# Performance work log

Hardware: AMD Instinct MI355X
Metric: run time of the kernel (lower is better)

Reference implementation:

```python
import jax, jax.numpy as jnp
import numpy as np

B, S, E, H = 1024, 64, 1024, 16  # batch, seq (n_agent+1), n_embd, num_heads
D = E // H  # head_dim = 64


def setup_inputs() -> dict:
    k = jax.random.key(0)
    ks = jax.random.split(k, 7)
    w = lambda i: jax.random.normal(ks[i], (E, E), jnp.float32) * 0.02
    return {
        "query": jax.random.normal(ks[0], (B, S, E), jnp.float32),
        "key": jax.random.normal(ks[1], (B, S, E), jnp.float32),
        "value": jax.random.normal(ks[2], (B, S, E), jnp.float32),
        "Wq": w(3), "bq": jnp.zeros((E,), jnp.float32),
        "Wk": w(4), "bk": jnp.zeros((E,), jnp.float32),
        "Wv": w(5), "bv": jnp.zeros((E,), jnp.float32),
        "Wo": w(6), "bo": jnp.zeros((E,), jnp.float32),
    }


def reference(query, key, value, Wq, bq, Wk, bk, Wv, bv, Wo, bo):
    Bq, Q, _ = query.shape
    K = key.shape[1]
    # projections -> [B, H, L, D]
    q = (query @ Wq + bq).reshape(Bq, Q, H, D).transpose(0, 2, 1, 3)
    k = (key @ Wk + bk).reshape(Bq, K, H, D).transpose(0, 2, 1, 3)
    v = (value @ Wv + bv).reshape(Bq, K, H, D).transpose(0, 2, 1, 3)
    # non-standard: ReLU on Q and K before scores
    q = jnp.maximum(q, 0.0)
    k = jnp.maximum(k, 0.0)
    scale = 1.0 / jnp.sqrt(jnp.float32(D))
    scores = jnp.einsum('bhqd,bhkd->bhqk', q, k) * scale  # [B,H,Q,K]
    # causal mask (tril of the (n_agent+1)^2 mask, sliced to q_len,kv_len)
    mask = jnp.tril(jnp.ones((Q, K), jnp.float32))[None, None]
    scores = jnp.where(mask == 0, jnp.finfo(jnp.float32).min, scores)
    attn = jax.nn.softmax(scores, axis=-1)
    out = jnp.einsum('bhqk,bhkd->bhqd', attn, v)
    out = out.transpose(0, 2, 1, 3).reshape(Bq, Q, E)
    return out @ Wo + bo
```

## Files before the change

kernel.cpp:

```cpp
#include <hip/hip_runtime.h>

typedef __attribute__((ext_vector_type(4))) float f32x4;
typedef __attribute__((ext_vector_type(8))) short short8;
typedef __attribute__((ext_vector_type(2))) unsigned int uint2v;
typedef __attribute__((ext_vector_type(4))) unsigned int uint4v;

#define MFMA_BF16(a,b,c) __builtin_amdgcn_mfma_f32_16x16x32_bf16(a,b,c,0,0,0)

__device__ __forceinline__ unsigned short bf16_of(float f) {
  union { float f; unsigned int u; } v; v.f = f;
  unsigned int r = v.u + 0x7fffu + ((v.u >> 16) & 1u);
  return (unsigned short)(r >> 16);
}

__device__ __forceinline__ unsigned int cvt_pk_bf16(float lo, float hi) {
  unsigned int r;
  asm("v_cvt_pk_bf16_f32 %0, %1, %2" : "=v"(r) : "v"(lo), "v"(hi));
  return r;
}

__device__ __forceinline__ void gload_lds16(const void* g, void* l) {
  __builtin_amdgcn_global_load_lds(
      (const __attribute__((address_space(1))) unsigned int*)g,
      (__attribute__((address_space(3))) unsigned int*)l, 16, 0, 0);
}

__global__ __launch_bounds__(256)
void wcast_kernel(const float* __restrict__ W0, const float* __restrict__ W1,
                  const float* __restrict__ W2, const float* __restrict__ W3,
                  unsigned short* __restrict__ wt) {
  __shared__ float tile[64][65];
  const float* W = (blockIdx.z == 0) ? W0 : (blockIdx.z == 1) ? W1
                 : (blockIdx.z == 2) ? W2 : W3;
  unsigned short* Wt = wt + (size_t)blockIdx.z * (1024u * 1024u);
  int k0 = blockIdx.x * 64, n0 = blockIdx.y * 64;
  int t = threadIdx.x, r = t >> 6, c = t & 63;
#pragma unroll
  for (int i = 0; i < 16; ++i)
    tile[r + i * 4][c] = W[(size_t)(k0 + r + i * 4) * 1024 + n0 + c];
  __syncthreads();
#pragma unroll
  for (int i = 0; i < 16; ++i)
    Wt[(size_t)(n0 + r + i * 4) * 1024 + k0 + c] = bf16_of(tile[c][r + i * 4]);
}

__global__ __launch_bounds__(512, 4)
void gemm_qkv(const float* __restrict__ Aq, const float* __restrict__ Ak,
              const float* __restrict__ Av, const unsigned short* __restrict__ wt,
              const float* __restrict__ bq, const float* __restrict__ bk,
              const float* __restrict__ bv, unsigned short* __restrict__ qw,
              unsigned short* __restrict__ kw, unsigned short* __restrict__ vw) {
  __shared__ unsigned short ldsA[128 * 64];
  __shared__ unsigned short ldsB[256 * 64];

  int z = blockIdx.z;
  const float* Af = (z == 0) ? Aq : (z == 1) ? Ak : Av;
  const unsigned short* Bt = wt + (size_t)z * 1048576;
  const float* bias = (z == 0) ? bq : (z == 1) ? bk : bv;
  unsigned short* C = (z == 0) ? qw : (z == 1) ? kw : vw;

  int bid = blockIdx.x;
  int mt = (bid & 7) * 64 + (bid >> 5);
  int nt = (bid >> 3) & 3;
  int m0 = mt * 128, n0 = nt * 256;

  int tid = threadIdx.x;
  int w = tid >> 6, l = tid & 63;
  int wm = w >> 2, wn = w & 3;
  int li = l & 15, grp = l >> 4;

  f32x4 acc[4][4] = {};

  int grow = l >> 3;
  int gseg = (l & 7) ^ grow;

  int rA = tid >> 2, q = tid & 3;

  f32x4 areg[4];
  auto loadA = [&](int kt) {
#pragma unroll
    for (int j = 0; j < 4; ++j)
      areg[j] = *(const f32x4*)(Af + (size_t)(m0 + rA) * 1024 + kt * 64 + q * 16 + j * 4);
  };

  loadA(0);

  for (int kt = 0; kt < 16; ++kt) {
    int k0 = kt * 64;
#pragma unroll
    for (int i = 0; i < 4; ++i) {
      int c = w * 4 + i;
      gload_lds16(Bt + (size_t)(n0 + 8 * c + grow) * 1024 + k0 + gseg * 8,
                  (char*)ldsB + c * 1024);
    }
    {
      uint4v w0, w1;
      w0[0] = cvt_pk_bf16(areg[0][0], areg[0][1]);
      w0[1] = cvt_pk_bf16(areg[0][2], areg[0][3]);
      w0[2] = cvt_pk_bf16(areg[1][0], areg[1][1]);
      w0[3] = cvt_pk_bf16(areg[1][2], areg[1][3]);
      w1[0] = cvt_pk_bf16(areg[2][0], areg[2][1]);
      w1[1] = cvt_pk_bf16(areg[2][2], areg[2][3]);
      w1[2] = cvt_pk_bf16(areg[3][0], areg[3][1]);
      w1[3] = cvt_pk_bf16(areg[3][2], areg[3][3]);
      *(uint4v*)((char*)ldsA + rA * 128 + (((2 * q)     ^ (rA & 7)) << 4)) = w0;
      *(uint4v*)((char*)ldsA + rA * 128 + (((2 * q + 1) ^ (rA & 7)) << 4)) = w1;
    }
    __syncthreads();
    if (kt < 15) {
      loadA(kt + 1);
      __builtin_amdgcn_sched_barrier(0);
    }
#pragma unroll
    for (int ks = 0; ks < 2; ++ks) {
      short8 af[4], bf[4];
#pragma unroll
      for (int mi = 0; mi < 4; ++mi) {
        int row = wm * 64 + mi * 16 + li;
        af[mi] = *(const short8*)((const char*)ldsA + row * 128 +
                                  (((ks * 4 + grp) ^ (row & 7)) << 4));
      }
#pragma unroll
      for (int ni = 0; ni < 4; ++ni) {
        int row = wn * 64 + ni * 16 + li;
        bf[ni] = *(const short8*)((const char*)ldsB + row * 128 +
                                  (((ks * 4 + grp) ^ (row & 7)) << 4));
      }
#pragma unroll
      for (int mi = 0; mi < 4; ++mi)
#pragma unroll
        for (int ni = 0; ni < 4; ++ni)
          acc[mi][ni] = MFMA_BF16(af[mi], bf[ni], acc[mi][ni]);
    }
    __syncthreads();
  }

  int mrow0 = m0 + wm * 64;
  int ncol0 = n0 + wn * 64;
  float bvv[4];
#pragma unroll
  for (int ni = 0; ni < 4; ++ni) bvv[ni] = bias[ncol0 + ni * 16 + li];

  int b = mrow0 >> 6, h = ncol0 >> 6;
  unsigned short* base = C + (size_t)b * 65536 + (size_t)h * 4096;
  if (z < 2) {
#pragma unroll
    for (int mi = 0; mi < 4; ++mi)
#pragma unroll
      for (int ni = 0; ni < 4; ++ni)
#pragma unroll
        for (int j = 0; j < 4; ++j) {
          float v = acc[mi][ni][j] + bvv[ni];
          v = fmaxf(v, 0.0f);
          base[(mi * 16 + grp * 4 + j) * 64 + ni * 16 + li] = bf16_of(v);
        }
  } else {
#pragma unroll
    for (int mi = 0; mi < 4; ++mi)
#pragma unroll
      for (int ni = 0; ni < 4; ++ni) {
        uint2v pk;
        pk.x = cvt_pk_bf16(acc[mi][ni][0] + bvv[ni], acc[mi][ni][1] + bvv[ni]);
        pk.y = cvt_pk_bf16(acc[mi][ni][2] + bvv[ni], acc[mi][ni][3] + bvv[ni]);
        *(uint2v*)(base + (ni * 16 + li) * 64 + mi * 16 + grp * 4) = pk;
      }
  }
}

__global__ __launch_bounds__(512, 4)
void gemm_out(const unsigned short* __restrict__ Ab, const unsigned short* __restrict__ Bt,
              const float* __restrict__ bias, float* __restrict__ C) {
  __shared__ unsigned short ldsA[128 * 64];
  __shared__ unsigned short ldsB[256 * 64];

  int bid = blockIdx.x;
  int mt = (bid & 7) * 64 + (bid >> 5);
  int nt = (bid >> 3) & 3;
  int m0 = mt * 128, n0 = nt * 256;

  int tid = threadIdx.x;
  int w = tid >> 6, l = tid & 63;
  int wm = w >> 2, wn = w & 3;
  int li = l & 15, grp = l >> 4;

  f32x4 acc[4][4] = {};

  int grow = l >> 3;
  int gseg = (l & 7) ^ grow;

  int rA = tid >> 2, q = tid & 3;

  short8 a0, a1;
  auto loadA = [&](int kt) {
    a0 = *(const short8*)(Ab + (size_t)(m0 + rA) * 1024 + kt * 64 + q * 16);
    a1 = *(const short8*)(Ab + (size_t)(m0 + rA) * 1024 + kt * 64 + q * 16 + 8);
  };

  loadA(0);

  for (int kt = 0; kt < 16; ++kt) {
    int k0 = kt * 64;
#pragma unroll
    for (int i = 0; i < 4; ++i) {
      int c = w * 4 + i;
      gload_lds16(Bt + (size_t)(n0 + 8 * c + grow) * 1024 + k0 + gseg * 8,
                  (char*)ldsB + c * 1024);
    }
    *(short8*)((char*)ldsA + rA * 128 + (((2 * q)     ^ (rA & 7)) << 4)) = a0;
    *(short8*)((char*)ldsA + rA * 128 + (((2 * q + 1) ^ (rA & 7)) << 4)) = a1;
    __syncthreads();
    if (kt < 15) {
      loadA(kt + 1);
      __builtin_amdgcn_sched_barrier(0);
    }
#pragma unroll
    for (int ks = 0; ks < 2; ++ks) {
      short8 af[4], bf[4];
#pragma unroll
      for (int mi = 0; mi < 4; ++mi) {
        int row = wm * 64 + mi * 16 + li;
        af[mi] = *(const short8*)((const char*)ldsA + row * 128 +
                                  (((ks * 4 + grp) ^ (row & 7)) << 4));
      }
#pragma unroll
      for (int ni = 0; ni < 4; ++ni) {
        int row = wn * 64 + ni * 16 + li;
        bf[ni] = *(const short8*)((const char*)ldsB + row * 128 +
                                  (((ks * 4 + grp) ^ (row & 7)) << 4));
      }
#pragma unroll
      for (int mi = 0; mi < 4; ++mi)
#pragma unroll
        for (int ni = 0; ni < 4; ++ni)
          acc[mi][ni] = MFMA_BF16(af[mi], bf[ni], acc[mi][ni]);
    }
    __syncthreads();
  }

  int mrow0 = m0 + wm * 64;
  int ncol0 = n0 + wn * 64;
  float bvv[4];
#pragma unroll
  for (int ni = 0; ni < 4; ++ni) bvv[ni] = bias[ncol0 + ni * 16 + li];
#pragma unroll
  for (int mi = 0; mi < 4; ++mi)
#pragma unroll
    for (int ni = 0; ni < 4; ++ni)
#pragma unroll
      for (int j = 0; j < 4; ++j)
        C[(size_t)(mrow0 + mi * 16 + grp * 4 + j) * 1024 + ncol0 + ni * 16 + li] =
            acc[mi][ni][j] + bvv[ni];
}

__global__ __launch_bounds__(64)
void attn_kernel(const unsigned short* __restrict__ qw,
                 const unsigned short* __restrict__ kw,
                 const unsigned short* __restrict__ vw,
                 unsigned short* __restrict__ aw) {
  __shared__ unsigned short p_lds[64 * 72];
  int bh = blockIdx.x;
  int b = bh >> 4, h = bh & 15;
  int l = threadIdx.x;
  int li = l & 15, grp = l >> 4;
  const unsigned short* qb = qw + (size_t)bh * 4096;
  const unsigned short* kb = kw + (size_t)bh * 4096;
  const unsigned short* vb = vw + (size_t)bh * 4096;

  short8 aq[4][2], bk_[4][2];
#pragma unroll
  for (int mi = 0; mi < 4; ++mi)
#pragma unroll
    for (int ks = 0; ks < 2; ++ks) {
      aq[mi][ks]  = *(const short8*)(qb + (mi * 16 + li) * 64 + ks * 32 + grp * 8);
      bk_[mi][ks] = *(const short8*)(kb + (mi * 16 + li) * 64 + ks * 32 + grp * 8);
    }

  f32x4 sf[4][4];
#pragma unroll
  for (int mi = 0; mi < 4; ++mi)
#pragma unroll
    for (int ni = 0; ni < 4; ++ni) {
      f32x4 t = {};
      t = MFMA_BF16(aq[mi][0], bk_[ni][0], t);
      t = MFMA_BF16(aq[mi][1], bk_[ni][1], t);
      sf[mi][ni] = t;
    }

#pragma unroll
  for (int mi = 0; mi < 4; ++mi) {
#pragma unroll
    for (int j = 0; j < 4; ++j) {
      int row = mi * 16 + grp * 4 + j;
      float mx = -1e30f;
#pragma unroll
      for (int ni = 0; ni < 4; ++ni) {
        int col = ni * 16 + li;
        float v = sf[mi][ni][j] * 0.125f;
        v = (col <= row) ? v : -1e30f;
        sf[mi][ni][j] = v;
        mx = fmaxf(mx, v);
      }
#pragma unroll
      for (int sh = 1; sh < 16; sh <<= 1) mx = fmaxf(mx, __shfl_xor(mx, sh, 64));
      float sum = 0.0f;
#pragma unroll
      for (int ni = 0; ni < 4; ++ni) {
        float e = __expf(sf[mi][ni][j] - mx);
        sf[mi][ni][j] = e;
        sum += e;
      }
#pragma unroll
      for (int sh = 1; sh < 16; sh <<= 1) sum += __shfl_xor(sum, sh, 64);
      float rr = 1.0f / sum;
#pragma unroll
      for (int ni = 0; ni < 4; ++ni) sf[mi][ni][j] *= rr;
    }
  }

#pragma unroll
  for (int mi = 0; mi < 4; ++mi)
#pragma unroll
    for (int ni = 0; ni < 4; ++ni)
#pragma unroll
      for (int j = 0; j < 4; ++j)
        p_lds[(mi * 16 + grp * 4 + j) * 72 + ni * 16 + li] = bf16_of(sf[mi][ni][j]);
  __syncthreads();

  short8 pa[4][2], bv_[4][2];
#pragma unroll
  for (int mi = 0; mi < 4; ++mi)
#pragma unroll
    for (int ks = 0; ks < 2; ++ks)
      pa[mi][ks] = *(const short8*)(p_lds + (mi * 16 + li) * 72 + ks * 32 + grp * 8);
#pragma unroll
  for (int ni = 0; ni < 4; ++ni)
#pragma unroll
    for (int ks = 0; ks < 2; ++ks)
      bv_[ni][ks] = *(const short8*)(vb + (ni * 16 + li) * 64 + ks * 32 + grp * 8);

  f32x4 of[4][4];
#pragma unroll
  for (int mi = 0; mi < 4; ++mi)
#pragma unroll
    for (int ni = 0; ni < 4; ++ni) {
      f32x4 t = {};
      t = MFMA_BF16(pa[mi][0], bv_[ni][0], t);
      t = MFMA_BF16(pa[mi][1], bv_[ni][1], t);
      of[mi][ni] = t;
    }

  unsigned short* ab = aw + (size_t)b * 65536 + (size_t)h * 64;
#pragma unroll
  for (int mi = 0; mi < 4; ++mi)
#pragma unroll
    for (int ni = 0; ni < 4; ++ni)
#pragma unroll
      for (int j = 0; j < 4; ++j)
        ab[(size_t)(mi * 16 + grp * 4 + j) * 1024 + ni * 16 + li] = bf16_of(of[mi][ni][j]);
}

extern "C" void kernel_launch(void* const* d_in, const int* in_sizes, int n_in,
                              void* d_out, int out_size, void* d_ws, size_t ws_size,
                              hipStream_t stream) {
  (void)in_sizes; (void)n_in; (void)out_size; (void)ws_size;
  const float* query = (const float*)d_in[0];
  const float* key   = (const float*)d_in[1];
  const float* value = (const float*)d_in[2];
  const float* Wq = (const float*)d_in[3];
  const float* bq = (const float*)d_in[4];
  const float* Wk = (const float*)d_in[5];
  const float* bk = (const float*)d_in[6];
  const float* Wv = (const float*)d_in[7];
  const float* bv = (const float*)d_in[8];
  const float* Wo = (const float*)d_in[9];
  const float* bo = (const float*)d_in[10];
  float* out = (float*)d_out;

  unsigned short* wt = (unsigned short*)d_ws;
  const size_t NE = (size_t)67108864;
  unsigned short* qw = wt + (size_t)4 * 1024 * 1024;
  unsigned short* kw = qw + NE;
  unsigned short* vw = kw + NE;
  unsigned short* aw = vw + NE;

  wcast_kernel<<<dim3(16, 16, 4), 256, 0, stream>>>(Wq, Wk, Wv, Wo, wt);
  gemm_qkv<<<dim3(2048, 1, 3), 512, 0, stream>>>(query, key, value, wt,
                                                 bq, bk, bv, qw, kw, vw);
  attn_kernel<<<dim3(16384), 64, 0, stream>>>(qw, kw, vw, aw);
  gemm_out<<<dim3(2048), 512, 0, stream>>>(aw, wt + (size_t)3 * 1048576, bo, out);
}
```

Measured before the change: 819.4 us.

## Double-buffer B tile in LDS to prefetch next k-tile during MFMA

Both projection GEMMs now keep two LDS buffers for the weight tile and issue the global-to-LDS load of the next k-step before the MFMA loop on the current one. The B-load latency can then overlap compute instead of sitting behind a barrier each iteration. The A tile stays single-buffered and is written after an extra barrier. The cost is more LDS per block (48KB to 80KB), which can reduce occupancy below the launch-bounds target, plus one more barrier per iteration.

Result: slower. 938.5 us (+14.5%).

```diff
diff --git a/kernel.cpp b/kernel.cpp
--- a/kernel.cpp
+++ b/kernel.cpp
@@ -51,7 +51,7 @@
               const float* __restrict__ bv, unsigned short* __restrict__ qw,
               unsigned short* __restrict__ kw, unsigned short* __restrict__ vw) {
   __shared__ unsigned short ldsA[128 * 64];
-  __shared__ unsigned short ldsB[256 * 64];
+  __shared__ unsigned short ldsB[2][256 * 64];
 
   int z = blockIdx.z;
   const float* Af = (z == 0) ? Aq : (z == 1) ? Ak : Av;
@@ -82,32 +82,37 @@
     for (int j = 0; j < 4; ++j)
       areg[j] = *(const f32x4*)(Af + (size_t)(m0 + rA) * 1024 + kt * 64 + q * 16 + j * 4);
   };
-
-  loadA(0);
-
-  for (int kt = 0; kt < 16; ++kt) {
-    int k0 = kt * 64;
+  auto writeA = [&]() {
+    uint4v w0, w1;
+    w0[0] = cvt_pk_bf16(areg[0][0], areg[0][1]);
+    w0[1] = cvt_pk_bf16(areg[0][2], areg[0][3]);
+    w0[2] = cvt_pk_bf16(areg[1][0], areg[1][1]);
+    w0[3] = cvt_pk_bf16(areg[1][2], areg[1][3]);
+    w1[0] = cvt_pk_bf16(areg[2][0], areg[2][1]);
+    w1[1] = cvt_pk_bf16(areg[2][2], areg[2][3]);
+    w1[2] = cvt_pk_bf16(areg[3][0], areg[3][1]);
+    w1[3] = cvt_pk_bf16(areg[3][2], areg[3][3]);
+    *(uint4v*)((char*)ldsA + rA * 128 + (((2 * q)     ^ (rA & 7)) << 4)) = w0;
+    *(uint4v*)((char*)ldsA + rA * 128 + (((2 * q + 1) ^ (rA & 7)) << 4)) = w1;
+  };
+  auto stageB = [&](int buf, int kt) {
 #pragma unroll
     for (int i = 0; i < 4; ++i) {
       int c = w * 4 + i;
-      gload_lds16(Bt + (size_t)(n0 + 8 * c + grow) * 1024 + k0 + gseg * 8,
-                  (char*)ldsB + c * 1024);
-    }
-    {
-      uint4v w0, w1;
-      w0[0] = cvt_pk_bf16(areg[0][0], areg[0][1]);
-      w0[1] = cvt_pk_bf16(areg[0][2], areg[0][3]);
-      w0[2] = cvt_pk_bf16(areg[1][0], areg[1][1]);
-      w0[3] = cvt_pk_bf16(areg[1][2], areg[1][3]);
-      w1[0] = cvt_pk_bf16(areg[2][0], areg[2][1]);
-      w1[1] = cvt_pk_bf16(areg[2][2], areg[2][3]);
-      w1[2] = cvt_pk_bf16(areg[3][0], areg[3][1]);
-      w1[3] = cvt_pk_bf16(areg[3][2], areg[3][3]);
-      *(uint4v*)((char*)ldsA + rA * 128 + (((2 * q)     ^ (rA & 7)) << 4)) = w0;
-      *(uint4v*)((char*)ldsA + rA * 128 + (((2 * q + 1) ^ (rA & 7)) << 4)) = w1;
-    }
-    __syncthreads();
+      gload_lds16(Bt + (size_t)(n0 + 8 * c + grow) * 1024 + kt * 64 + gseg * 8,
+                  (char*)&ldsB[buf][0] + c * 1024);
+    }
+  };
+
+  loadA(0);
+  writeA();
+  stageB(0, 0);
+  __syncthreads();
+
+  for (int kt = 0; kt < 16; ++kt) {
+    int cur = kt & 1;
     if (kt < 15) {
+      stageB(cur ^ 1, kt + 1);
       loadA(kt + 1);
       __builtin_amdgcn_sched_barrier(0);
     }
@@ -123,7 +128,7 @@
 #pragma unroll
       for (int ni = 0; ni < 4; ++ni) {
         int row = wn * 64 + ni * 16 + li;
-        bf[ni] = *(const short8*)((const char*)ldsB + row * 128 +
+        bf[ni] = *(const short8*)((const char*)&ldsB[cur][0] + row * 128 +
                                   (((ks * 4 + grp) ^ (row & 7)) << 4));
       }
 #pragma unroll
@@ -133,6 +138,10 @@
           acc[mi][ni] = MFMA_BF16(af[mi], bf[ni], acc[mi][ni]);
     }
     __syncthreads();
+    if (kt < 15) {
+      writeA();
+      __syncthreads();
+    }
   }
 
   int mrow0 = m0 + wm * 64;
@@ -171,7 +180,7 @@
 void gemm_out(const unsigned short* __restrict__ Ab, const unsigned short* __restrict__ Bt,
               const float* __restrict__ bias, float* __restrict__ C) {
   __shared__ unsigned short ldsA[128 * 64];
-  __shared__ unsigned short ldsB[256 * 64];
+  __shared__ unsigned short ldsB[2][256 * 64];
 
   int bid = blockIdx.x;
   int mt = (bid & 7) * 64 + (bid >> 5);
@@ -195,21 +204,28 @@
     a0 = *(const short8*)(Ab + (size_t)(m0 + rA) * 1024 + kt * 64 + q * 16);
     a1 = *(const short8*)(Ab + (size_t)(m0 + rA) * 1024 + kt * 64 + q * 16 + 8);
   };
-
-  loadA(0);
-
-  for (int kt = 0; kt < 16; ++kt) {
-    int k0 = kt * 64;
+  auto writeA = [&]() {
+    *(short8*)((char*)ldsA + rA * 128 + (((2 * q)     ^ (rA & 7)) << 4)) = a0;
+    *(short8*)((char*)ldsA + rA * 128 + (((2 * q + 1) ^ (rA & 7)) << 4)) = a1;
+  };
+  auto stageB = [&](int buf, int kt) {
 #pragma unroll
     for (int i = 0; i < 4; ++i) {
       int c = w * 4 + i;
-      gload_lds16(Bt + (size_t)(n0 + 8 * c + grow) * 1024 + k0 + gseg * 8,
-                  (char*)ldsB + c * 1024);
-    }
-    *(short8*)((char*)ldsA + rA * 128 + (((2 * q)     ^ (rA & 7)) << 4)) = a0;
-    *(short8*)((char*)ldsA + rA * 128 + (((2 * q + 1) ^ (rA & 7)) << 4)) = a1;
-    __syncthreads();
+      gload_lds16(Bt + (size_t)(n0 + 8 * c + grow) * 1024 + kt * 64 + gseg * 8,
+                  (char*)&ldsB[buf][0] + c * 1024);
+    }
+  };
+
+  loadA(0);
+  writeA();
+  stageB(0, 0);
+  __syncthreads();
+
+  for (int kt = 0; kt < 16; ++kt) {
+    int cur = kt & 1;
     if (kt < 15) {
+      stageB(cur ^ 1, kt + 1);
       loadA(kt + 1);
       __builtin_amdgcn_sched_barrier(0);
     }
@@ -225,7 +241,7 @@
 #pragma unroll
       for (int ni = 0; ni < 4; ++ni) {
         int row = wn * 64 + ni * 16 + li;
-        bf[ni] = *(const short8*)((const char*)ldsB + row * 128 +
+        bf[ni] = *(const short8*)((const char*)&ldsB[cur][0] + row * 128 +
                                   (((ks * 4 + grp) ^ (row & 7)) << 4));
       }
 #pragma unroll
@@ -235,6 +251,10 @@
           acc[mi][ni] = MFMA_BF16(af[mi], bf[ni], acc[mi][ni]);
     }
     __syncthreads();
+    if (kt < 15) {
+      writeA();
+      __syncthreads();
+    }
   }
 
   int mrow0 = m0 + wm * 64;
```
